# Kernel optimization log

Measured on AMD Instinct MI355X. Metric: run time of the kernel, lower is better.

Reference implementation:

```python
import jax, jax.numpy as jnp
import numpy as np

B, T, D = 2, 1024, 2048
HK, HV, DK, DV = 16, 32, 128, 128
KCONV = 4
INTER = 8192
EPS = 1e-6
KEY_DIM = HK * DK          # 2048
VAL_DIM = HV * DV          # 4096
CONV_DIM = 2 * KEY_DIM + VAL_DIM  # 8192


def setup_inputs() -> dict:
    key = jax.random.key(0)
    ks = jax.random.split(key, 16)
    s = 0.02
    return {
        "positions": jnp.broadcast_to(jnp.arange(T, dtype=jnp.int32), (B, T)),
        "hidden_states": jax.random.normal(ks[0], (B, T, D), jnp.float32),
        "residual": jax.random.normal(ks[1], (B, T, D), jnp.float32),
        "ln_in_w": jnp.zeros((D,), jnp.float32),
        "ln_post_w": jnp.zeros((D,), jnp.float32),
        "Wqkvz": jax.random.normal(ks[2], (D, 2 * KEY_DIM + 2 * VAL_DIM), jnp.float32) * s,
        "Wba": jax.random.normal(ks[3], (D, 2 * HV), jnp.float32) * s,
        "conv_w": jax.random.normal(ks[4], (CONV_DIM, KCONV), jnp.float32) * 0.1,
        "A_log": jnp.log(jax.random.uniform(ks[5], (HV,), jnp.float32, 1.0, 16.0)),
        "dt_bias": jax.random.normal(ks[6], (HV,), jnp.float32) * 0.1,
        "norm_w": jnp.ones((DV,), jnp.float32),
        "Wout": jax.random.normal(ks[7], (VAL_DIM, D), jnp.float32) * s,
        "Wgate": jax.random.normal(ks[8], (D, INTER), jnp.float32) * s,
        "Wup": jax.random.normal(ks[9], (D, INTER), jnp.float32) * s,
        "Wdown": jax.random.normal(ks[10], (INTER, D), jnp.float32) * s,
    }


def _gemma_rmsnorm(x, w):
    xf = x.astype(jnp.float32)
    v = jnp.mean(xf * xf, axis=-1, keepdims=True)
    return (xf * jax.lax.rsqrt(v + EPS) * (1.0 + w)).astype(x.dtype)


def _causal_depthwise_conv(x, w):
    # x: [B,T,C], w: [C,K]; causal depthwise conv1d
    Kw = w.shape[1]
    Tlen = x.shape[1]
    xp = jnp.pad(x, ((0, 0), (Kw - 1, 0), (0, 0)))
    return sum(xp[:, i:i + Tlen, :] * w[:, i] for i in range(Kw))


def _l2norm(x):
    return x * jax.lax.rsqrt(jnp.sum(x * x, axis=-1, keepdims=True) + 1e-6)


def reference(positions, hidden_states, residual, ln_in_w, ln_post_w, Wqkvz, Wba,
              conv_w, A_log, dt_bias, norm_w, Wout, Wgate, Wup, Wdown):
    b, t, d = hidden_states.shape
    # fused input RMSNorm + residual add
    res1 = hidden_states + residual
    h = _gemma_rmsnorm(res1, ln_in_w)

    # ---- GatedDeltaNet linear attention ----
    qkvz = h @ Wqkvz
    q, k, v, z = jnp.split(qkvz, [KEY_DIM, 2 * KEY_DIM, 2 * KEY_DIM + VAL_DIM], axis=-1)
    ba = h @ Wba
    bb, aa = jnp.split(ba, [HV], axis=-1)  # [b,t,HV] each

    qkv = jax.nn.silu(_causal_depthwise_conv(jnp.concatenate([q, k, v], axis=-1), conv_w))
    q, k, v = jnp.split(qkv, [KEY_DIM, 2 * KEY_DIM], axis=-1)

    q = _l2norm(q.reshape(b, t, HK, DK))
    k = _l2norm(k.reshape(b, t, HK, DK))
    v = v.reshape(b, t, HV, DV)
    z = z.reshape(b, t, HV, DV)
    rep = HV // HK
    q = jnp.repeat(q, rep, axis=2) * (DK ** -0.5)  # [b,t,HV,DK]
    k = jnp.repeat(k, rep, axis=2)

    beta = jax.nn.sigmoid(bb)                              # [b,t,HV]
    decay = jnp.exp(-jnp.exp(A_log) * jax.nn.softplus(aa + dt_bias))  # [b,t,HV]

    def step(S, xs):
        q_t, k_t, v_t, b_t, d_t = xs  # [b,HV,DK],[b,HV,DK],[b,HV,DV],[b,HV],[b,HV]
        S = S * d_t[..., None, None]
        v_pred = jnp.einsum('bhk,bhkv->bhv', k_t, S)
        delta = (v_t - v_pred) * b_t[..., None]
        S = S + jnp.einsum('bhk,bhv->bhkv', k_t, delta)
        o = jnp.einsum('bhk,bhkv->bhv', q_t, S)
        return S, o

    xs = (q.transpose(1, 0, 2, 3), k.transpose(1, 0, 2, 3), v.transpose(1, 0, 2, 3),
          beta.transpose(1, 0, 2), decay.transpose(1, 0, 2))
    S0 = jnp.zeros((b, HV, DK, DV), dtype=q.dtype)
    _, o = jax.lax.scan(step, S0, xs)
    o = o.transpose(1, 0, 2, 3)  # [b,t,HV,DV]

    # gated per-head RMSNorm: gate first (Qwen3-Next style), then normalize
    og = (o * jax.nn.silu(z)).astype(jnp.float32)
    var = jnp.mean(og * og, axis=-1, keepdims=True)
    og = (og * jax.lax.rsqrt(var + EPS)) * norm_w
    attn = og.reshape(b, t, VAL_DIM).astype(h.dtype) @ Wout

    # fused post-attention RMSNorm + residual
    res2 = attn + res1
    h2 = _gemma_rmsnorm(res2, ln_post_w)

    # gated SiLU MLP
    out = (jax.nn.silu(h2 @ Wgate) * (h2 @ Wup)) @ Wdown
    return (out, res2)
```

## Files before the change

kernel.cpp:

```cpp
#include <hip/hip_runtime.h>
#include <hip/hip_bf16.h>

typedef unsigned short u16;
typedef unsigned int u32;
typedef float f32x4 __attribute__((ext_vector_type(4)));
typedef short bf16x8 __attribute__((ext_vector_type(8)));
typedef unsigned short u16x4 __attribute__((ext_vector_type(4)));
typedef unsigned int u32x2 __attribute__((ext_vector_type(2)));
typedef unsigned int u32x4 __attribute__((ext_vector_type(4)));

#define BT 2048
#define DMODEL 2048
#define HV 32
#define DK 128
#define KEYDIM 2048
#define VALDIM 4096
#define QKVZ_N 12288
#define CONVC 8192
#define INTER 8192

__device__ __forceinline__ float bf2f(u16 v) {
  u32 u = ((u32)v) << 16;
  return __builtin_bit_cast(float, u);
}
__device__ __forceinline__ u16 f2bf(float f) {
  u32 u = __builtin_bit_cast(u32, f);
  u32 r = (u + 0x7fffu + ((u >> 16) & 1u)) >> 16;
  return (u16)r;
}
__device__ __forceinline__ u32 pack2(float a, float b) {
  return (u32)f2bf(a) | ((u32)f2bf(b) << 16);
}
__device__ __forceinline__ float siluf(float x) {
  return x / (1.f + expf(-x));
}

__global__ __launch_bounds__(256) void convert_transpose(
    const float* __restrict__ W, int ldw, u16* __restrict__ Wt, int K, int N) {
  __shared__ float tileT[64][68];
  int n0 = blockIdx.x * 64, k0 = blockIdx.y * 64;
  int tx = threadIdx.x & 15, ty = threadIdx.x >> 4;
#pragma unroll
  for (int i = 0; i < 4; ++i) {
    int kk = ty + i * 16;
    f32x4 v = *(const f32x4*)(W + (size_t)(k0 + kk) * ldw + n0 + tx * 4);
#pragma unroll
    for (int j = 0; j < 4; ++j) tileT[tx * 4 + j][kk] = v[j];
  }
  __syncthreads();
#pragma unroll
  for (int i = 0; i < 4; ++i) {
    int nn = ty + i * 16;
    f32x4 v = *(const f32x4*)(&tileT[nn][tx * 4]);
    u16x4 st;
#pragma unroll
    for (int j = 0; j < 4; ++j) st[j] = f2bf(v[j]);
    *(u16x4*)(Wt + (size_t)(n0 + nn) * K + k0 + tx * 4) = st;
  }
}

__global__ __launch_bounds__(256) void resnorm_kernel(
    const float* __restrict__ a, const float* __restrict__ b,
    const float* __restrict__ w, float* __restrict__ resout,
    u16* __restrict__ hb) {
  int tok = blockIdx.x, t = threadIdx.x;
  const float* ap = a + (size_t)tok * DMODEL + t * 8;
  const float* bp = b + (size_t)tok * DMODEL + t * 8;
  f32x4 x0 = *(const f32x4*)ap + *(const f32x4*)bp;
  f32x4 x1 = *(const f32x4*)(ap + 4) + *(const f32x4*)(bp + 4);
  *(f32x4*)(resout + (size_t)tok * DMODEL + t * 8) = x0;
  *(f32x4*)(resout + (size_t)tok * DMODEL + t * 8 + 4) = x1;
  float ss = 0.f;
#pragma unroll
  for (int j = 0; j < 4; ++j) ss += x0[j] * x0[j] + x1[j] * x1[j];
#pragma unroll
  for (int m = 1; m < 64; m <<= 1) ss += __shfl_xor(ss, m, 64);
  __shared__ float red[4];
  if ((t & 63) == 0) red[t >> 6] = ss;
  __syncthreads();
  ss = red[0] + red[1] + red[2] + red[3];
  float sc = rsqrtf(ss * (1.f / (float)DMODEL) + 1e-6f);
  const float* wp = w + t * 8;
  float y[8];
#pragma unroll
  for (int j = 0; j < 4; ++j) {
    y[j] = x0[j] * sc * (1.f + wp[j]);
    y[4 + j] = x1[j] * sc * (1.f + wp[4 + j]);
  }
  u32x4 st;
  st[0] = pack2(y[0], y[1]);
  st[1] = pack2(y[2], y[3]);
  st[2] = pack2(y[4], y[5]);
  st[3] = pack2(y[6], y[7]);
  *(u32x4*)(hb + (size_t)tok * DMODEL + t * 8) = st;
}

__global__ __launch_bounds__(256) void resnorm2_kernel(
    const float* __restrict__ p, const float* __restrict__ b,
    const float* __restrict__ w, float* __restrict__ resout,
    u16* __restrict__ hb) {
  int tok = blockIdx.x, t = threadIdx.x;
  size_t base = (size_t)tok * DMODEL + t * 8;
  const float* p0 = p + base;
  const float* p1 = p + (size_t)BT * DMODEL + base;
  const float* bp = b + base;
  f32x4 x0 = *(const f32x4*)p0 + *(const f32x4*)p1 + *(const f32x4*)bp;
  f32x4 x1 = *(const f32x4*)(p0 + 4) + *(const f32x4*)(p1 + 4) +
             *(const f32x4*)(bp + 4);
  *(f32x4*)(resout + base) = x0;
  *(f32x4*)(resout + base + 4) = x1;
  float ss = 0.f;
#pragma unroll
  for (int j = 0; j < 4; ++j) ss += x0[j] * x0[j] + x1[j] * x1[j];
#pragma unroll
  for (int m = 1; m < 64; m <<= 1) ss += __shfl_xor(ss, m, 64);
  __shared__ float red[4];
  if ((t & 63) == 0) red[t >> 6] = ss;
  __syncthreads();
  ss = red[0] + red[1] + red[2] + red[3];
  float sc = rsqrtf(ss * (1.f / (float)DMODEL) + 1e-6f);
  const float* wp = w + t * 8;
  float y[8];
#pragma unroll
  for (int j = 0; j < 4; ++j) {
    y[j] = x0[j] * sc * (1.f + wp[j]);
    y[4 + j] = x1[j] * sc * (1.f + wp[4 + j]);
  }
  u32x4 st;
  st[0] = pack2(y[0], y[1]);
  st[1] = pack2(y[2], y[3]);
  st[2] = pack2(y[4], y[5]);
  st[3] = pack2(y[6], y[7]);
  *(u32x4*)(hb + base) = st;
}

__device__ __forceinline__ void async16(const void* g, void* l) {
  __builtin_amdgcn_global_load_lds(
      (const __attribute__((address_space(1))) u32*)g,
      (__attribute__((address_space(3))) u32*)l, 16, 0, 0);
}

template <int OUT>
__global__ __launch_bounds__(256) void gemm_kernel(
    const u16* __restrict__ A, const u16* __restrict__ Bt,
    void* __restrict__ Cv, const u16* __restrict__ Aux, int M, int N,
    int Kfull, int Ks) {
  __shared__ __align__(16) u16 Al[4][128 * 32];
  __shared__ __align__(16) u16 Bl[4][128 * 32];
  int tid = threadIdx.x;
  int w = tid >> 6, l = tid & 63;
  int wr = w >> 1, wc = w & 1;
  int r15 = l & 15, kb = l >> 4;

  int nbx = gridDim.x, nby = gridDim.y;
  int bid = blockIdx.y * nbx + blockIdx.x;
  int nwg = nbx * nby;
  int cpx = nwg >> 3;
  int wg = (bid & 7) * cpx + (bid >> 3);
  const int GRP = 4;
  int span = GRP * nby;
  int grpId = wg / span;
  int rem = wg - grpId * span;
  int n0 = (grpId * GRP + (rem % GRP)) * 128;
  int m0 = (rem / GRP) * 128;
  int kbase = blockIdx.z * Ks;

  f32x4 acc[4][4] = {};

  const u16* baseA[2];
  const u16* baseB[2];
#pragma unroll
  for (int c = 0; c < 2; ++c) {
    int gid = w * 128 + c * 64 + l;
    int row = gid >> 2;
    int g = (gid & 3) ^ ((row >> 1) & 3);
    baseA[c] = A + (size_t)(m0 + row) * Kfull + kbase + g * 8;
    baseB[c] = Bt + (size_t)(n0 + row) * Kfull + kbase + g * 8;
  }
  auto stage = [&](int buf, int koff) {
#pragma unroll
    for (int c = 0; c < 2; ++c) {
      int gid = w * 128 + c * 64 + l;
      async16(baseA[c] + koff, Al[buf] + gid * 8);
      async16(baseB[c] + koff, Bl[buf] + gid * 8);
    }
  };

  int nst = Ks >> 5;
#pragma unroll
  for (int p = 0; p < 3; ++p)
    if (p < nst) stage(p & 3, p * 32);

  for (int i = 0; i < nst; ++i) {
    int issued = (i + 3 < nst) ? (i + 3) : nst;
    int infl = issued - i - 1;
    if (infl >= 2)
      asm volatile("s_waitcnt vmcnt(8)" ::: "memory");
    else if (infl == 1)
      asm volatile("s_waitcnt vmcnt(4)" ::: "memory");
    else
      asm volatile("s_waitcnt vmcnt(0)" ::: "memory");
    __builtin_amdgcn_s_barrier();
    __builtin_amdgcn_sched_barrier(0);
    if (i + 3 < nst) stage((i + 3) & 3, (i + 3) * 32);
    const u16* Ac = Al[i & 3];
    const u16* Bc = Bl[i & 3];
    bf16x8 aF[4], bF[4];
#pragma unroll
    for (int m = 0; m < 4; ++m) {
      int row = wr * 64 + m * 16 + r15;
      aF[m] = *(const bf16x8*)(Ac + row * 32 + (kb ^ ((row >> 1) & 3)) * 8);
    }
#pragma unroll
    for (int n = 0; n < 4; ++n) {
      int row = wc * 64 + n * 16 + r15;
      bF[n] = *(const bf16x8*)(Bc + row * 32 + (kb ^ ((row >> 1) & 3)) * 8);
    }
#pragma unroll
    for (int m = 0; m < 4; ++m)
#pragma unroll
      for (int n = 0; n < 4; ++n)
        acc[m][n] = __builtin_amdgcn_mfma_f32_16x16x32_bf16(aF[m], bF[n],
                                                            acc[m][n], 0, 0, 0);
  }

  float* Cf = (float*)Cv + (size_t)blockIdx.z * M * N;
#pragma unroll
  for (int m = 0; m < 4; ++m)
#pragma unroll
    for (int n = 0; n < 4; ++n) {
      size_t base = (size_t)(m0 + wr * 64 + m * 16 + kb * 4) * N +
                    (n0 + wc * 64 + n * 16 + r15);
#pragma unroll
      for (int r = 0; r < 4; ++r) {
        size_t idx = base + (size_t)r * N;
        if (OUT == 0)
          Cf[idx] = acc[m][n][r];
        else if (OUT == 1)
          ((u16*)Cv)[idx] = f2bf(acc[m][n][r]);
        else
          ((u16*)Cv)[idx] = f2bf(siluf(bf2f(Aux[idx])) * acc[m][n][r]);
      }
    }
}

#define GPHASE(ACHUNK, BCHUNK, Q, READ_B, ST_OP, ST_KH, TAILVM)              \
  {                                                                          \
    if (READ_B) {                                                            \
      _Pragma("unroll") for (int n = 0; n < 4; ++n) {                        \
        int row = wn * 64 + n * 16 + r15;                                    \
        bF[n] = *(const bf16x8*)((BCHUNK) + row * 32 +                       \
                                 (kb ^ ((row >> 1) & 3)) * 8);               \
      }                                                                      \
    }                                                                        \
    _Pragma("unroll") for (int mm = 0; mm < 4; ++mm) {                       \
      int row = wm * 128 + (Q)*64 + mm * 16 + r15;                           \
      aF[mm] = *(const bf16x8*)((ACHUNK) + row * 32 +                        \
                                (kb ^ ((row >> 1) & 3)) * 8);                \
    }                                                                        \
    if (hn) stage(buf ^ 1, ST_OP, ST_KH, koff);                              \
    __builtin_amdgcn_s_barrier();                                            \
    asm volatile("s_waitcnt lgkmcnt(0)" ::: "memory");                       \
    __builtin_amdgcn_sched_barrier(0);                                       \
    __builtin_amdgcn_s_setprio(1);                                           \
    _Pragma("unroll") for (int mm = 0; mm < 4; ++mm)                         \
        _Pragma("unroll") for (int n = 0; n < 4; ++n)                        \
            acc[(Q)*4 + mm][n] = __builtin_amdgcn_mfma_f32_16x16x32_bf16(    \
                aF[mm], bF[n], acc[(Q)*4 + mm][n], 0, 0, 0);                 \
    __builtin_amdgcn_s_setprio(0);                                           \
    if (TAILVM) {                                                            \
      if (hn)                                                                \
        asm volatile("s_waitcnt vmcnt(4)" ::: "memory");                     \
      else                                                                   \
        asm volatile("s_waitcnt vmcnt(0)" ::: "memory");                     \
    }                                                                        \
    __builtin_amdgcn_s_barrier();                                            \
  }

template <int OUT>
__global__ __launch_bounds__(512, 2) void gemm256_kernel(
    const u16* __restrict__ A, const u16* __restrict__ Bt,
    void* __restrict__ Cv, const u16* __restrict__ Aux, int M, int N,
    int Kfull, int Ks) {
  __shared__ __align__(16) u16 S[65536];
  int tid = threadIdx.x;
  int l = tid & 63, w = tid >> 6;
  int wm = w >> 2, wn = w & 3;
  int r15 = l & 15, kb = l >> 4;

  int nbx = gridDim.x, nby = gridDim.y;
  int bid = blockIdx.y * nbx + blockIdx.x;
  int nwg = nbx * nby;
  int cpx = nwg >> 3;
  int wg = (bid & 7) * cpx + (bid >> 3);
  const int GRP = 4;
  int span = GRP * nby;
  int grpId = wg / span;
  int rem = wg - grpId * span;
  int n0 = (grpId * GRP + (rem % GRP)) * 256;
  int m0 = (rem / GRP) * 256;
  int kbase = blockIdx.z * Ks;

  f32x4 acc[8][4] = {};

  const u16* baseA[2];
  const u16* baseB[2];
#pragma unroll
  for (int c = 0; c < 2; ++c) {
    int gid = c * 512 + tid;
    int row = gid >> 2, gg = gid & 3;
    int gl = gg ^ ((row >> 1) & 3);
    baseA[c] = A + (size_t)(m0 + row) * Kfull + kbase + gl * 8;
    baseB[c] = Bt + (size_t)(n0 + row) * Kfull + kbase + gl * 8;
  }
  auto stage = [&](int buf, int op, int kh, int koff) {
#pragma unroll
    for (int c = 0; c < 2; ++c) {
      int gid = c * 512 + tid;
      const u16* src = (op == 0 ? baseA[c] : baseB[c]) + koff + kh * 32;
      async16(src, S + ((buf * 2 + op) * 2 + kh) * 8192 + gid * 8);
    }
  };

  int nt = Ks >> 6;
  stage(0, 0, 0, 0);
  stage(0, 1, 0, 0);
  stage(0, 0, 1, 0);
  stage(0, 1, 1, 0);
  asm volatile("s_waitcnt vmcnt(4)" ::: "memory");
  __builtin_amdgcn_s_barrier();

  for (int t = 0; t < nt; ++t) {
    int buf = t & 1;
    bool hn = t + 1 < nt;
    int koff = (t + 1) * 64;
    const u16* Ac0 = S + ((buf * 2 + 0) * 2 + 0) * 8192;
    const u16* Ac1 = S + ((buf * 2 + 0) * 2 + 1) * 8192;
    const u16* Bc0 = S + ((buf * 2 + 1) * 2 + 0) * 8192;
    const u16* Bc1 = S + ((buf * 2 + 1) * 2 + 1) * 8192;
    bf16x8 aF[4], bF[4];
    GPHASE(Ac0, Bc0, 0, true, 0, 0, false)
    GPHASE(Ac0, Bc0, 1, false, 1, 0, true)
    GPHASE(Ac1, Bc1, 0, true, 0, 1, false)
    GPHASE(Ac1, Bc1, 1, false, 1, 1, true)
  }

  float* Cf = (float*)Cv + (size_t)blockIdx.z * M * N;
#pragma unroll
  for (int m = 0; m < 8; ++m)
#pragma unroll
    for (int n = 0; n < 4; ++n) {
      size_t base = (size_t)(m0 + wm * 128 + m * 16 + kb * 4) * N +
                    (n0 + wn * 64 + n * 16 + r15);
#pragma unroll
      for (int r = 0; r < 4; ++r) {
        size_t idx = base + (size_t)r * N;
        if (OUT == 0)
          Cf[idx] = acc[m][n][r];
        else if (OUT == 1)
          ((u16*)Cv)[idx] = f2bf(acc[m][n][r]);
        else
          ((u16*)Cv)[idx] = f2bf(siluf(bf2f(Aux[idx])) * acc[m][n][r]);
      }
    }
}

__global__ __launch_bounds__(256) void reduce_kernel(
    const float* __restrict__ p, float* __restrict__ o, int n, int S) {
  int i = (blockIdx.x * 256 + threadIdx.x) * 4;
  f32x4 s = *(const f32x4*)(p + i);
  for (int j = 1; j < S; ++j) s += *(const f32x4*)(p + (size_t)j * n + i);
  *(f32x4*)(o + i) = s;
}

__global__ __launch_bounds__(256) void ba_gemm_kernel(
    const u16* __restrict__ hb, const float* __restrict__ Wba,
    float* __restrict__ ba) {
  int m = blockIdx.x;
  int t = threadIdx.x;
  int n = t & 63, kq = t >> 6;
  const u16* a = hb + (size_t)m * DMODEL + kq * 512;
  const float* wp = Wba + (size_t)kq * 512 * 64 + n;
  float sum = 0.f;
  for (int i = 0; i < 512; ++i)
    sum += bf2f(a[i]) * wp[(size_t)i * 64];
  __shared__ float red[256];
  red[t] = sum;
  __syncthreads();
  if (t < 64)
    ba[(size_t)m * 64 + t] = red[t] + red[t + 64] + red[t + 128] + red[t + 192];
}

__global__ __launch_bounds__(256) void conv_silu_kernel(
    const u16* __restrict__ qkvb, const float* __restrict__ conv_w,
    u16* __restrict__ qkv) {
  int gid = blockIdx.x * 256 + threadIdx.x;
  int c4 = (gid & 2047) * 4;
  int bt = gid >> 11;
  int b = bt >> 10, tt = bt & 1023;
  f32x4 wv[4];
#pragma unroll
  for (int j = 0; j < 4; ++j) wv[j] = *(const f32x4*)(conv_w + (c4 + j) * 4);
  float acc[4] = {0.f, 0.f, 0.f, 0.f};
#pragma unroll
  for (int i = 0; i < 4; ++i) {
    int ts = tt - 3 + i;
    if (ts >= 0) {
      u16x4 x = *(const u16x4*)(qkvb + (size_t)(b * 1024 + ts) * CONVC + c4);
#pragma unroll
      for (int j = 0; j < 4; ++j) acc[j] += bf2f(x[j]) * wv[j][i];
    }
  }
  u32x2 st;
  st[0] = pack2(siluf(acc[0]), siluf(acc[1]));
  st[1] = pack2(siluf(acc[2]), siluf(acc[3]));
  *(u32x2*)(qkv + (size_t)bt * CONVC + c4) = st;
}

__global__ __launch_bounds__(256) void l2norm_kernel(u16* __restrict__ qkv) {
  int wid = blockIdx.x * 4 + (threadIdx.x >> 6);
  int l = threadIdx.x & 63;
  int tok = wid >> 5, slot = wid & 31;
  u16* p = qkv + (size_t)tok * CONVC + slot * 128 + l * 2;
  float x0 = bf2f(p[0]), x1 = bf2f(p[1]);
  float ss = x0 * x0 + x1 * x1;
#pragma unroll
  for (int m = 1; m < 64; m <<= 1) ss += __shfl_xor(ss, m, 64);
  float sc = rsqrtf(ss + 1e-6f);
  if (slot < 16) sc *= 0.08838834764831845f;
  *(u32*)p = pack2(x0 * sc, x1 * sc);
}

__global__ __launch_bounds__(256) void betadecay_kernel(
    const float* __restrict__ ba, const float* __restrict__ A_log,
    const float* __restrict__ dt_bias, float* __restrict__ bd) {
  int idx = blockIdx.x * 256 + threadIdx.x;
  int h = idx & 31;
  int tok = idx >> 5;
  int b = tok >> 10, tt = tok & 1023;
  float bb = ba[(size_t)tok * 64 + h];
  float aa = ba[(size_t)tok * 64 + 32 + h];
  float bet = 1.f / (1.f + expf(-bb));
  float x = aa + dt_bias[h];
  float sp = (x > 20.f) ? x : log1pf(expf(x));
  float dec = expf(-expf(A_log[h]) * sp);
  size_t o = (((size_t)(b * 32 + h)) * 1024 + tt) * 2;
  bd[o] = bet;
  bd[o + 1] = dec;
}

__global__ __launch_bounds__(256) void prep_kernel(
    const u16* __restrict__ qkvc, const float* __restrict__ bdpack,
    u16* __restrict__ Tg, u16* __restrict__ Pg, u16* __restrict__ KtTg,
    float* __restrict__ Bvec) {
  __shared__ __align__(16) u16 Kl[64 * 128];
  __shared__ __align__(16) u16 Ql[64 * 128];
  __shared__ __align__(16) float Af[64 * 65];
  __shared__ float bl[64], betal[64], sc63[64];
  int tid = threadIdx.x;
  int w = tid >> 6, l = tid & 63;
  int r15 = l & 15, kb = l >> 4;
  int c = blockIdx.x, bh = blockIdx.y;
  int b = bh >> 5, h = bh & 31, hk = h >> 1;
  size_t tok0 = (size_t)b * 1024 + c * 64;
  int ch = bh * 16 + c;

#pragma unroll
  for (int rep = 0; rep < 4; ++rep) {
    int gid = w * 256 + rep * 64 + l;
    int row = gid >> 4, seg = gid & 15;
    const u16* srcq = qkvc + (tok0 + row) * CONVC + hk * 128 + seg * 8;
    async16(srcq, Ql + gid * 8);
    async16(srcq + KEYDIM, Kl + gid * 8);
  }
  if (tid < 64) {
    size_t o = ((size_t)bh * 1024 + c * 64 + tid) * 2;
    betal[tid] = bdpack[o];
    float s = logf(fmaxf(bdpack[o + 1], 1e-30f));
#pragma unroll
    for (int d = 1; d < 64; d <<= 1) {
      float t = __shfl_up(s, d, 64);
      if (tid >= d) s += t;
    }
    bl[tid] = s;
    float tot = __shfl(s, 63, 64);
    sc63[tid] = expf(tot - s);
    Bvec[(size_t)ch * 64 + tid] = expf(s);
  }
  __syncthreads();

  {
    f32x4 akk[4] = {}, aqk[4] = {};
#pragma unroll
    for (int ks = 0; ks < 4; ++ks) {
      bf16x8 kaF = *(const bf16x8*)(Kl + (w * 16 + r15) * 128 + ks * 32 + kb * 8);
      bf16x8 qaF = *(const bf16x8*)(Ql + (w * 16 + r15) * 128 + ks * 32 + kb * 8);
#pragma unroll
      for (int n = 0; n < 4; ++n) {
        bf16x8 bF = *(const bf16x8*)(Kl + (n * 16 + r15) * 128 + ks * 32 + kb * 8);
        akk[n] = __builtin_amdgcn_mfma_f32_16x16x32_bf16(kaF, bF, akk[n], 0, 0, 0);
        aqk[n] = __builtin_amdgcn_mfma_f32_16x16x32_bf16(qaF, bF, aqk[n], 0, 0, 0);
      }
    }
#pragma unroll
    for (int n = 0; n < 4; ++n)
#pragma unroll
      for (int r = 0; r < 4; ++r) {
        int i = w * 16 + kb * 4 + r;
        int j = n * 16 + r15;
        float e = expf(bl[i] - bl[j]);
        Af[i * 65 + j] = (j < i) ? betal[i] * e * akk[n][r] : 0.f;
        u16 pv = (j <= i) ? f2bf(e * aqk[n][r]) : (u16)0;
        Pg[(size_t)ch * 4096 + i * 64 + j] = pv;
      }
  }
  for (int m = 0; m < 32; ++m) {
    int idx = tid * 32 + m;
    int d = idx >> 6, j = idx & 63;
    KtTg[(size_t)ch * 8192 + idx] = f2bf(bf2f(Kl[j * 128 + d]) * sc63[j]);
  }
  __syncthreads();

  {
    int ccol = w * 16 + r15;
    float tj[16];
#pragma unroll
    for (int m = 0; m < 16; ++m) tj[m] = (4 * m + kb == ccol) ? 1.f : 0.f;
#pragma unroll
    for (int i = 1; i < 64; ++i) {
      float part = 0.f;
      const int mb = (i + 3) >> 2;
#pragma unroll
      for (int m = 0; m < 16; ++m)
        if (m < mb) part = fmaf(Af[i * 65 + 4 * m + kb], tj[m], part);
      part += __shfl_xor(part, 16, 64);
      part += __shfl_xor(part, 32, 64);
      float nv = ((ccol == i) ? 1.f : 0.f) - part;
      if (kb == (i & 3)) tj[i >> 2] = nv;
    }
#pragma unroll
    for (int m = 0; m < 16; ++m)
      Tg[(size_t)ch * 4096 + (4 * m + kb) * 64 + ccol] = f2bf(tj[m]);
  }
}

__global__ __launch_bounds__(512) void chunk_scan_kernel(
    const u16* __restrict__ qkvc, const float* __restrict__ bdpack,
    const u16* __restrict__ Tg, const u16* __restrict__ Pg,
    const u16* __restrict__ KtTg, const float* __restrict__ Bvec,
    u16* __restrict__ obf) {
  __shared__ __align__(16) u16 Kl[64 * 128];
  __shared__ __align__(16) u16 Ql[64 * 128];
  __shared__ __align__(16) u16 KtTl[128 * 64];
  __shared__ __align__(16) u16 Tl[64 * 64];
  __shared__ __align__(16) u16 Pl[64 * 64];
  __shared__ __align__(16) u16 Vl[64 * 32];
  __shared__ __align__(16) u16 St[32 * 128];
  __shared__ __align__(16) u16 rhsT[32 * 64];
  __shared__ __align__(16) u16 dT[32 * 64];
  __shared__ float betal[64], Gl[64];

  int tid = threadIdx.x;
  int w = tid >> 6, l = tid & 63;
  int r15 = l & 15, kb = l >> 4;
  int dvc = blockIdx.x, bh = blockIdx.y;
  int b = bh >> 5, h = bh & 31, hk = h >> 1;
  int a = w >> 1, bcol = w & 1;

  for (int m = tid; m < 32 * 128; m += 512) St[m] = 0;
  f32x4 sAcc0 = {}, sAcc1 = {};
  __syncthreads();

  for (int c = 0; c < 16; ++c) {
    size_t tok0 = (size_t)b * 1024 + c * 64;
    int ch = bh * 16 + c;
#pragma unroll
    for (int rep = 0; rep < 2; ++rep) {
      int gid = w * 128 + rep * 64 + l;
      int row = gid >> 4, seg = gid & 15;
      const u16* srcq = qkvc + (tok0 + row) * CONVC + hk * 128 + seg * 8;
      async16(srcq, Ql + gid * 8);
      async16(srcq + KEYDIM, Kl + gid * 8);
      async16(KtTg + (size_t)ch * 8192 + gid * 8, KtTl + gid * 8);
    }
    {
      int gid = w * 64 + l;
      async16(Tg + (size_t)ch * 4096 + gid * 8, Tl + gid * 8);
      async16(Pg + (size_t)ch * 4096 + gid * 8, Pl + gid * 8);
    }
    if (w < 4) {
      int gid = w * 64 + l;
      int row = gid >> 2, seg = gid & 3;
      async16(qkvc + (tok0 + row) * CONVC + 2 * KEYDIM + h * 128 + dvc * 32 + seg * 8,
              Vl + gid * 8);
    }
    if (tid < 64) {
      betal[tid] = bdpack[((size_t)bh * 1024 + c * 64 + tid) * 2];
      Gl[tid] = Bvec[(size_t)ch * 64 + tid];
    }
    __syncthreads();

    f32x4 aKS = {}, aQS = {};
#pragma unroll
    for (int ks = 0; ks < 4; ++ks) {
      bf16x8 bF = *(const bf16x8*)(St + (bcol * 16 + r15) * 128 + ks * 32 + kb * 8);
      bf16x8 kF = *(const bf16x8*)(Kl + (a * 16 + r15) * 128 + ks * 32 + kb * 8);
      bf16x8 qF = *(const bf16x8*)(Ql + (a * 16 + r15) * 128 + ks * 32 + kb * 8);
      aKS = __builtin_amdgcn_mfma_f32_16x16x32_bf16(kF, bF, aKS, 0, 0, 0);
      aQS = __builtin_amdgcn_mfma_f32_16x16x32_bf16(qF, bF, aQS, 0, 0, 0);
    }
    {
      int i0 = a * 16 + kb * 4;
      int dv = bcol * 16 + r15;
      u16x4 st;
#pragma unroll
      for (int r = 0; r < 4; ++r) {
        int i = i0 + r;
        float v = bf2f(Vl[i * 32 + dv]);
        st[r] = f2bf(betal[i] * (v - Gl[i] * aKS[r]));
      }
      *(u16x4*)(rhsT + dv * 64 + i0) = st;
    }
    __syncthreads();
    f32x4 aD = {};
#pragma unroll
    for (int ks = 0; ks < 2; ++ks) {
      bf16x8 aF = *(const bf16x8*)(Tl + (a * 16 + r15) * 64 + ks * 32 + kb * 8);
      bf16x8 bF = *(const bf16x8*)(rhsT + (bcol * 16 + r15) * 64 + ks * 32 + kb * 8);
      aD = __builtin_amdgcn_mfma_f32_16x16x32_bf16(aF, bF, aD, 0, 0, 0);
    }
    {
      int i0 = a * 16 + kb * 4;
      int dv = bcol * 16 + r15;
      u16x4 st;
#pragma unroll
      for (int r = 0; r < 4; ++r) st[r] = f2bf(aD[r]);
      *(u16x4*)(dT + dv * 64 + i0) = st;
    }
    __syncthreads();
    f32x4 aO = {};
#pragma unroll
    for (int ks = 0; ks < 2; ++ks) {
      bf16x8 aF = *(const bf16x8*)(Pl + (a * 16 + r15) * 64 + ks * 32 + kb * 8);
      bf16x8 bF = *(const bf16x8*)(dT + (bcol * 16 + r15) * 64 + ks * 32 + kb * 8);
      aO = __builtin_amdgcn_mfma_f32_16x16x32_bf16(aF, bF, aO, 0, 0, 0);
    }
    {
      int i0 = a * 16 + kb * 4;
      int dv = bcol * 16 + r15;
#pragma unroll
      for (int r = 0; r < 4; ++r) {
        int i = i0 + r;
        float o = aO[r] + Gl[i] * aQS[r];
        obf[(tok0 + i) * VALDIM + h * 128 + dvc * 32 + dv] = f2bf(o);
      }
    }
    float gL = Gl[63];
#pragma unroll
    for (int r = 0; r < 4; ++r) { sAcc0[r] *= gL; sAcc1[r] *= gL; }
#pragma unroll
    for (int ks = 0; ks < 2; ++ks) {
      bf16x8 aF = *(const bf16x8*)(KtTl + (w * 16 + r15) * 64 + ks * 32 + kb * 8);
      bf16x8 b0 = *(const bf16x8*)(dT + r15 * 64 + ks * 32 + kb * 8);
      bf16x8 b1 = *(const bf16x8*)(dT + (16 + r15) * 64 + ks * 32 + kb * 8);
      sAcc0 = __builtin_amdgcn_mfma_f32_16x16x32_bf16(aF, b0, sAcc0, 0, 0, 0);
      sAcc1 = __builtin_amdgcn_mfma_f32_16x16x32_bf16(aF, b1, sAcc1, 0, 0, 0);
    }
#pragma unroll
    for (int r = 0; r < 4; ++r) {
      int dk = w * 16 + kb * 4 + r;
      St[r15 * 128 + dk] = f2bf(sAcc0[r]);
      St[(16 + r15) * 128 + dk] = f2bf(sAcc1[r]);
    }
    __syncthreads();
  }
}

__global__ __launch_bounds__(256) void gatenorm_kernel(
    const u16* __restrict__ obf, u16* __restrict__ zb,
    const float* __restrict__ norm_w) {
  int wid = blockIdx.x * 4 + (threadIdx.x >> 6);
  int l = threadIdx.x & 63;
  int tok = wid >> 5, h = wid & 31;
  const u16* op = obf + (size_t)tok * VALDIM + h * 128 + l * 2;
  u16* zp = zb + (size_t)tok * VALDIM + h * 128 + l * 2;
  float o0 = bf2f(op[0]), o1 = bf2f(op[1]);
  float z0 = bf2f(zp[0]), z1 = bf2f(zp[1]);
  float g0 = o0 * siluf(z0);
  float g1 = o1 * siluf(z1);
  float ss = g0 * g0 + g1 * g1;
#pragma unroll
  for (int m = 1; m < 64; m <<= 1) ss += __shfl_xor(ss, m, 64);
  float sc = rsqrtf(ss * (1.f / 128.f) + 1e-6f);
  int e = l * 2;
  *(u32*)zp = pack2(g0 * sc * norm_w[e], g1 * sc * norm_w[e + 1]);
}

__global__ void diag_kernel(float* out, float val) { out[0] = val; }

extern "C" void kernel_launch(void* const* d_in, const int* in_sizes, int n_in,
                              void* d_out, int out_size, void* d_ws,
                              size_t ws_size, hipStream_t stream) {
  const float* hidden = (const float*)d_in[1];
  const float* residual = (const float*)d_in[2];
  const float* ln_in_w = (const float*)d_in[3];
  const float* ln_post_w = (const float*)d_in[4];
  const float* Wqkvz = (const float*)d_in[5];
  const float* Wba = (const float*)d_in[6];
  const float* conv_w = (const float*)d_in[7];
  const float* A_log = (const float*)d_in[8];
  const float* dt_bias = (const float*)d_in[9];
  const float* norm_w = (const float*)d_in[10];
  const float* Wout = (const float*)d_in[11];
  const float* Wgate = (const float*)d_in[12];
  const float* Wup = (const float*)d_in[13];
  const float* Wdown = (const float*)d_in[14];

  char* ws = (char*)d_ws;
  size_t off = 0;
  auto alloc = [&](size_t n) {
    char* p = ws + off;
    off = (off + n + 255) & ~(size_t)255;
    return p;
  };
  u16* wslot = (u16*)alloc((size_t)INTER * DMODEL * 2);
  u16* hb = (u16*)alloc((size_t)BT * DMODEL * 2);
  u16* qkvb = (u16*)alloc((size_t)BT * CONVC * 2);
  u16* zb = (u16*)alloc((size_t)BT * VALDIM * 2);
  u16* qkvc = (u16*)alloc((size_t)BT * CONVC * 2);
  float* ba = (float*)alloc((size_t)BT * 64 * 4);
  float* bdpack = (float*)alloc((size_t)64 * 1024 * 2 * 4);
  u16* obf = (u16*)alloc((size_t)BT * VALDIM * 2);
  if (off > ws_size) {
    diag_kernel<<<1, 1, 0, stream>>>((float*)d_out, (float)(ws_size >> 20));
    return;
  }

  float* res1 = (float*)d_out;
  float* res2 = (float*)d_out + (size_t)BT * DMODEL;
  u16* h2b = hb;
  u16* gbuf = qkvc;
  u16* mbuf = qkvb;
  float* outp = (float*)d_out;

  u16* Tg = qkvb;
  u16* Pg = qkvb + (size_t)1024 * 4096;
  u16* KtTg = qkvb + (size_t)2 * 1024 * 4096;
  float* Bvec = ba;

  float* pWout = (float*)qkvb;
  float* pDown = (float*)zb;

  dim3 blk(256);
  dim3 blk512(512);

  resnorm_kernel<<<BT, blk, 0, stream>>>(hidden, residual, ln_in_w, res1, hb);

  convert_transpose<<<dim3(CONVC / 64, DMODEL / 64), blk, 0, stream>>>(
      Wqkvz, QKVZ_N, wslot, DMODEL, CONVC);
  gemm256_kernel<1><<<dim3(CONVC / 256, BT / 256), blk512, 0, stream>>>(
      hb, wslot, qkvb, nullptr, BT, CONVC, DMODEL, DMODEL);

  convert_transpose<<<dim3(VALDIM / 64, DMODEL / 64), blk, 0, stream>>>(
      Wqkvz + CONVC, QKVZ_N, wslot, DMODEL, VALDIM);
  gemm_kernel<1><<<dim3(VALDIM / 128, BT / 128), blk, 0, stream>>>(
      hb, wslot, zb, nullptr, BT, VALDIM, DMODEL, DMODEL);

  ba_gemm_kernel<<<BT, blk, 0, stream>>>(hb, Wba, ba);

  conv_silu_kernel<<<BT * 2048 / 256, blk, 0, stream>>>(qkvb, conv_w, qkvc);
  l2norm_kernel<<<BT * 32 / 4, blk, 0, stream>>>(qkvc);
  betadecay_kernel<<<BT * HV / 256, blk, 0, stream>>>(ba, A_log, dt_bias,
                                                      bdpack);

  prep_kernel<<<dim3(16, 64), blk, 0, stream>>>(qkvc, bdpack, Tg, Pg, KtTg,
                                                Bvec);
  chunk_scan_kernel<<<dim3(4, 64), dim3(512), 0, stream>>>(
      qkvc, bdpack, Tg, Pg, KtTg, Bvec, obf);

  gatenorm_kernel<<<BT * HV / 4, blk, 0, stream>>>(obf, zb, norm_w);

  convert_transpose<<<dim3(DMODEL / 64, VALDIM / 64), blk, 0, stream>>>(
      Wout, DMODEL, wslot, VALDIM, DMODEL);
  gemm_kernel<0><<<dim3(DMODEL / 128, BT / 128, 2), blk, 0, stream>>>(
      zb, wslot, pWout, nullptr, BT, DMODEL, VALDIM, VALDIM / 2);

  resnorm2_kernel<<<BT, blk, 0, stream>>>(pWout, res1, ln_post_w, res2, h2b);

  convert_transpose<<<dim3(INTER / 64, DMODEL / 64), blk, 0, stream>>>(
      Wgate, INTER, wslot, DMODEL, INTER);
  gemm256_kernel<1><<<dim3(INTER / 256, BT / 256), blk512, 0, stream>>>(
      h2b, wslot, gbuf, nullptr, BT, INTER, DMODEL, DMODEL);

  convert_transpose<<<dim3(INTER / 64, DMODEL / 64), blk, 0, stream>>>(
      Wup, INTER, wslot, DMODEL, INTER);
  gemm256_kernel<2><<<dim3(INTER / 256, BT / 256), blk512, 0, stream>>>(
      h2b, wslot, mbuf, gbuf, BT, INTER, DMODEL, DMODEL);

  convert_transpose<<<dim3(DMODEL / 64, INTER / 64), blk, 0, stream>>>(
      Wdown, DMODEL, wslot, INTER, DMODEL);
  gemm256_kernel<0><<<dim3(DMODEL / 256, BT / 256, 4), blk512, 0, stream>>>(
      mbuf, wslot, pDown, nullptr, BT, DMODEL, INTER, INTER / 4);
  reduce_kernel<<<BT * DMODEL / 1024, blk, 0, stream>>>(pDown, outp,
                                                        BT * DMODEL, 4);
}
```

Baseline: 764.4 us.

## Use 1024-thread GEMM tiles and fuse conv/l2norm and ba/betadecay kernels

The 256x256 GEMM now runs with 1024 threads (16 waves, each holding a 64x64 accumulator) instead of 512 threads, with one async load per operand per half-k and a simpler barrier schedule. Separately, causal conv+SiLU and per-head L2 norm are fused into one per-token kernel, and the beta/alpha projection is fused with the beta/decay computation, which removes intermediate buffers and launches. The Bvec buffer gets its own allocation instead of aliasing ba. The risks are register or LDS pressure and occupancy changes in the GEMM, plus a 256-thread per-token conv kernel that keeps 32 accumulators per thread.

```diff
diff --git a/kernel.cpp b/kernel.cpp
--- a/kernel.cpp
+++ b/kernel.cpp
@@ -244,41 +244,8 @@
     }
 }
 
-#define GPHASE(ACHUNK, BCHUNK, Q, READ_B, ST_OP, ST_KH, TAILVM)              \
-  {                                                                          \
-    if (READ_B) {                                                            \
-      _Pragma("unroll") for (int n = 0; n < 4; ++n) {                        \
-        int row = wn * 64 + n * 16 + r15;                                    \
-        bF[n] = *(const bf16x8*)((BCHUNK) + row * 32 +                       \
-                                 (kb ^ ((row >> 1) & 3)) * 8);               \
-      }                                                                      \
-    }                                                                        \
-    _Pragma("unroll") for (int mm = 0; mm < 4; ++mm) {                       \
-      int row = wm * 128 + (Q)*64 + mm * 16 + r15;                           \
-      aF[mm] = *(const bf16x8*)((ACHUNK) + row * 32 +                        \
-                                (kb ^ ((row >> 1) & 3)) * 8);                \
-    }                                                                        \
-    if (hn) stage(buf ^ 1, ST_OP, ST_KH, koff);                              \
-    __builtin_amdgcn_s_barrier();                                            \
-    asm volatile("s_waitcnt lgkmcnt(0)" ::: "memory");                       \
-    __builtin_amdgcn_sched_barrier(0);                                       \
-    __builtin_amdgcn_s_setprio(1);                                           \
-    _Pragma("unroll") for (int mm = 0; mm < 4; ++mm)                         \
-        _Pragma("unroll") for (int n = 0; n < 4; ++n)                        \
-            acc[(Q)*4 + mm][n] = __builtin_amdgcn_mfma_f32_16x16x32_bf16(    \
-                aF[mm], bF[n], acc[(Q)*4 + mm][n], 0, 0, 0);                 \
-    __builtin_amdgcn_s_setprio(0);                                           \
-    if (TAILVM) {                                                            \
-      if (hn)                                                                \
-        asm volatile("s_waitcnt vmcnt(4)" ::: "memory");                     \
-      else                                                                   \
-        asm volatile("s_waitcnt vmcnt(0)" ::: "memory");                     \
-    }                                                                        \
-    __builtin_amdgcn_s_barrier();                                            \
-  }
-
 template <int OUT>
-__global__ __launch_bounds__(512, 2) void gemm256_kernel(
+__global__ __launch_bounds__(1024, 1) void gemm1024_kernel(
     const u16* __restrict__ A, const u16* __restrict__ Bt,
     void* __restrict__ Cv, const u16* __restrict__ Aux, int M, int N,
     int Kfull, int Ks) {
@@ -301,56 +268,71 @@
   int m0 = (rem / GRP) * 256;
   int kbase = blockIdx.z * Ks;
 
-  f32x4 acc[8][4] = {};
-
-  const u16* baseA[2];
-  const u16* baseB[2];
-#pragma unroll
-  for (int c = 0; c < 2; ++c) {
-    int gid = c * 512 + tid;
-    int row = gid >> 2, gg = gid & 3;
-    int gl = gg ^ ((row >> 1) & 3);
-    baseA[c] = A + (size_t)(m0 + row) * Kfull + kbase + gl * 8;
-    baseB[c] = Bt + (size_t)(n0 + row) * Kfull + kbase + gl * 8;
-  }
-  auto stage = [&](int buf, int op, int kh, int koff) {
-#pragma unroll
-    for (int c = 0; c < 2; ++c) {
-      int gid = c * 512 + tid;
-      const u16* src = (op == 0 ? baseA[c] : baseB[c]) + koff + kh * 32;
-      async16(src, S + ((buf * 2 + op) * 2 + kh) * 8192 + gid * 8);
-    }
-  };
+  f32x4 acc[4][4] = {};
+
+  int srow = tid >> 2, sgg = tid & 3;
+  int sgl = sgg ^ ((srow >> 1) & 3);
+  const u16* baseA = A + (size_t)(m0 + srow) * Kfull + kbase + sgl * 8;
+  const u16* baseB = Bt + (size_t)(n0 + srow) * Kfull + kbase + sgl * 8;
 
   int nt = Ks >> 6;
-  stage(0, 0, 0, 0);
-  stage(0, 1, 0, 0);
-  stage(0, 0, 1, 0);
-  stage(0, 1, 1, 0);
-  asm volatile("s_waitcnt vmcnt(4)" ::: "memory");
+#pragma unroll
+  for (int kh = 0; kh < 2; ++kh) {
+    async16(baseA + kh * 32, S + ((0 * 2 + 0) * 2 + kh) * 8192 + tid * 8);
+    async16(baseB + kh * 32, S + ((0 * 2 + 1) * 2 + kh) * 8192 + tid * 8);
+  }
+  asm volatile("s_waitcnt vmcnt(2)" ::: "memory");
   __builtin_amdgcn_s_barrier();
 
   for (int t = 0; t < nt; ++t) {
     int buf = t & 1;
     bool hn = t + 1 < nt;
     int koff = (t + 1) * 64;
-    const u16* Ac0 = S + ((buf * 2 + 0) * 2 + 0) * 8192;
-    const u16* Ac1 = S + ((buf * 2 + 0) * 2 + 1) * 8192;
-    const u16* Bc0 = S + ((buf * 2 + 1) * 2 + 0) * 8192;
-    const u16* Bc1 = S + ((buf * 2 + 1) * 2 + 1) * 8192;
-    bf16x8 aF[4], bF[4];
-    GPHASE(Ac0, Bc0, 0, true, 0, 0, false)
-    GPHASE(Ac0, Bc0, 1, false, 1, 0, true)
-    GPHASE(Ac1, Bc1, 0, true, 0, 1, false)
-    GPHASE(Ac1, Bc1, 1, false, 1, 1, true)
+#pragma unroll
+    for (int kh = 0; kh < 2; ++kh) {
+      const u16* Ac = S + ((buf * 2 + 0) * 2 + kh) * 8192;
+      const u16* Bc = S + ((buf * 2 + 1) * 2 + kh) * 8192;
+      bf16x8 aF[4], bF[4];
+#pragma unroll
+      for (int m = 0; m < 4; ++m) {
+        int row = wm * 64 + m * 16 + r15;
+        aF[m] = *(const bf16x8*)(Ac + row * 32 + (kb ^ ((row >> 1) & 3)) * 8);
+      }
+#pragma unroll
+      for (int n = 0; n < 4; ++n) {
+        int row = wn * 64 + n * 16 + r15;
+        bF[n] = *(const bf16x8*)(Bc + row * 32 + (kb ^ ((row >> 1) & 3)) * 8);
+      }
+      if (hn) {
+        async16(baseA + koff + kh * 32,
+                S + (((buf ^ 1) * 2 + 0) * 2 + kh) * 8192 + tid * 8);
+        async16(baseB + koff + kh * 32,
+                S + (((buf ^ 1) * 2 + 1) * 2 + kh) * 8192 + tid * 8);
+      }
+      asm volatile("s_waitcnt lgkmcnt(0)" ::: "memory");
+      __builtin_amdgcn_sched_barrier(0);
+      __builtin_amdgcn_s_setprio(1);
+#pragma unroll
+      for (int m = 0; m < 4; ++m)
+#pragma unroll
+        for (int n = 0; n < 4; ++n)
+          acc[m][n] = __builtin_amdgcn_mfma_f32_16x16x32_bf16(
+              aF[m], bF[n], acc[m][n], 0, 0, 0);
+      __builtin_amdgcn_s_setprio(0);
+      if (hn)
+        asm volatile("s_waitcnt vmcnt(2)" ::: "memory");
+      else if (kh == 0)
+        asm volatile("s_waitcnt vmcnt(0)" ::: "memory");
+      __builtin_amdgcn_s_barrier();
+    }
   }
 
   float* Cf = (float*)Cv + (size_t)blockIdx.z * M * N;
 #pragma unroll
-  for (int m = 0; m < 8; ++m)
+  for (int m = 0; m < 4; ++m)
 #pragma unroll
     for (int n = 0; n < 4; ++n) {
-      size_t base = (size_t)(m0 + wm * 128 + m * 16 + kb * 4) * N +
+      size_t base = (size_t)(m0 + wm * 64 + m * 16 + kb * 4) * N +
                     (n0 + wn * 64 + n * 16 + r15);
 #pragma unroll
       for (int r = 0; r < 4; ++r) {
@@ -373,9 +355,10 @@
   *(f32x4*)(o + i) = s;
 }
 
-__global__ __launch_bounds__(256) void ba_gemm_kernel(
+__global__ __launch_bounds__(256) void ba_bd_kernel(
     const u16* __restrict__ hb, const float* __restrict__ Wba,
-    float* __restrict__ ba) {
+    const float* __restrict__ A_log, const float* __restrict__ dt_bias,
+    float* __restrict__ bd) {
   int m = blockIdx.x;
   int t = threadIdx.x;
   int n = t & 63, kq = t >> 6;
@@ -387,66 +370,72 @@
   __shared__ float red[256];
   red[t] = sum;
   __syncthreads();
-  if (t < 64)
-    ba[(size_t)m * 64 + t] = red[t] + red[t + 64] + red[t + 128] + red[t + 192];
-}
-
-__global__ __launch_bounds__(256) void conv_silu_kernel(
+  if (t < 32) {
+    float bb = red[t] + red[t + 64] + red[t + 128] + red[t + 192];
+    float aa = red[t + 32] + red[t + 96] + red[t + 160] + red[t + 224];
+    float bet = 1.f / (1.f + expf(-bb));
+    float x = aa + dt_bias[t];
+    float sp = (x > 20.f) ? x : log1pf(expf(x));
+    float dec = expf(-expf(A_log[t]) * sp);
+    int b = m >> 10, tt = m & 1023;
+    size_t o = (((size_t)(b * 32 + t)) * 1024 + tt) * 2;
+    bd[o] = bet;
+    bd[o + 1] = dec;
+  }
+}
+
+__global__ __launch_bounds__(256) void conv_l2_kernel(
     const u16* __restrict__ qkvb, const float* __restrict__ conv_w,
     u16* __restrict__ qkv) {
-  int gid = blockIdx.x * 256 + threadIdx.x;
-  int c4 = (gid & 2047) * 4;
-  int bt = gid >> 11;
-  int b = bt >> 10, tt = bt & 1023;
-  f32x4 wv[4];
-#pragma unroll
-  for (int j = 0; j < 4; ++j) wv[j] = *(const f32x4*)(conv_w + (c4 + j) * 4);
-  float acc[4] = {0.f, 0.f, 0.f, 0.f};
-#pragma unroll
-  for (int i = 0; i < 4; ++i) {
-    int ts = tt - 3 + i;
-    if (ts >= 0) {
-      u16x4 x = *(const u16x4*)(qkvb + (size_t)(b * 1024 + ts) * CONVC + c4);
-#pragma unroll
-      for (int j = 0; j < 4; ++j) acc[j] += bf2f(x[j]) * wv[j][i];
-    }
-  }
-  u32x2 st;
-  st[0] = pack2(siluf(acc[0]), siluf(acc[1]));
-  st[1] = pack2(siluf(acc[2]), siluf(acc[3]));
-  *(u32x2*)(qkv + (size_t)bt * CONVC + c4) = st;
-}
-
-__global__ __launch_bounds__(256) void l2norm_kernel(u16* __restrict__ qkv) {
-  int wid = blockIdx.x * 4 + (threadIdx.x >> 6);
-  int l = threadIdx.x & 63;
-  int tok = wid >> 5, slot = wid & 31;
-  u16* p = qkv + (size_t)tok * CONVC + slot * 128 + l * 2;
-  float x0 = bf2f(p[0]), x1 = bf2f(p[1]);
-  float ss = x0 * x0 + x1 * x1;
-#pragma unroll
-  for (int m = 1; m < 64; m <<= 1) ss += __shfl_xor(ss, m, 64);
-  float sc = rsqrtf(ss + 1e-6f);
-  if (slot < 16) sc *= 0.08838834764831845f;
-  *(u32*)p = pack2(x0 * sc, x1 * sc);
-}
-
-__global__ __launch_bounds__(256) void betadecay_kernel(
-    const float* __restrict__ ba, const float* __restrict__ A_log,
-    const float* __restrict__ dt_bias, float* __restrict__ bd) {
-  int idx = blockIdx.x * 256 + threadIdx.x;
-  int h = idx & 31;
-  int tok = idx >> 5;
+  int tok = blockIdx.x;
   int b = tok >> 10, tt = tok & 1023;
-  float bb = ba[(size_t)tok * 64 + h];
-  float aa = ba[(size_t)tok * 64 + 32 + h];
-  float bet = 1.f / (1.f + expf(-bb));
-  float x = aa + dt_bias[h];
-  float sp = (x > 20.f) ? x : log1pf(expf(x));
-  float dec = expf(-expf(A_log[h]) * sp);
-  size_t o = (((size_t)(b * 32 + h)) * 1024 + tt) * 2;
-  bd[o] = bet;
-  bd[o + 1] = dec;
+  int t = threadIdx.x;
+  int c0 = t * 32;
+  float acc[32];
+  {
+    bf16x8 x[4][4];
+    bool valid[4];
+#pragma unroll
+    for (int i = 0; i < 4; ++i) {
+      int ts = tt - 3 + i;
+      valid[i] = ts >= 0;
+      const u16* rp = qkvb + (size_t)(b * 1024 + (valid[i] ? ts : 0)) * CONVC + c0;
+#pragma unroll
+      for (int gq = 0; gq < 4; ++gq) x[i][gq] = *(const bf16x8*)(rp + gq * 8);
+    }
+#pragma unroll
+    for (int gq = 0; gq < 4; ++gq)
+#pragma unroll
+      for (int j = 0; j < 8; ++j) {
+        f32x4 wv = *(const f32x4*)(conv_w + (c0 + gq * 8 + j) * 4);
+        float s = 0.f;
+#pragma unroll
+        for (int i = 0; i < 4; ++i)
+          if (valid[i]) s = fmaf(bf2f((u16)x[i][gq][j]), wv[i], s);
+        acc[gq * 8 + j] = siluf(s);
+      }
+  }
+  if (t < 128) {
+    float ss = 1e-6f;
+#pragma unroll
+    for (int j = 0; j < 32; ++j) ss += acc[j] * acc[j];
+    ss += __shfl_xor(ss, 1, 64);
+    ss += __shfl_xor(ss, 2, 64);
+    ss -= 3e-6f;
+    float sc = rsqrtf(ss);
+    if (t < 64) sc *= 0.08838834764831845f;
+#pragma unroll
+    for (int j = 0; j < 32; ++j) acc[j] *= sc;
+  }
+  u16* op = qkv + (size_t)tok * CONVC + c0;
+#pragma unroll
+  for (int gq = 0; gq < 4; ++gq) {
+    u32x4 st;
+#pragma unroll
+    for (int p2 = 0; p2 < 4; ++p2)
+      st[p2] = pack2(acc[gq * 8 + p2 * 2], acc[gq * 8 + p2 * 2 + 1]);
+    *(u32x4*)(op + gq * 8) = st;
+  }
 }
 
 __global__ __launch_bounds__(256) void prep_kernel(
@@ -728,7 +717,7 @@
   u16* qkvb = (u16*)alloc((size_t)BT * CONVC * 2);
   u16* zb = (u16*)alloc((size_t)BT * VALDIM * 2);
   u16* qkvc = (u16*)alloc((size_t)BT * CONVC * 2);
-  float* ba = (float*)alloc((size_t)BT * 64 * 4);
+  float* Bvec = (float*)alloc((size_t)1024 * 64 * 4);
   float* bdpack = (float*)alloc((size_t)64 * 1024 * 2 * 4);
   u16* obf = (u16*)alloc((size_t)BT * VALDIM * 2);
   if (off > ws_size) {
@@ -746,19 +735,18 @@
   u16* Tg = qkvb;
   u16* Pg = qkvb + (size_t)1024 * 4096;
   u16* KtTg = qkvb + (size_t)2 * 1024 * 4096;
-  float* Bvec = ba;
 
   float* pWout = (float*)qkvb;
   float* pDown = (float*)zb;
 
   dim3 blk(256);
-  dim3 blk512(512);
+  dim3 blk1024(1024);
 
   resnorm_kernel<<<BT, blk, 0, stream>>>(hidden, residual, ln_in_w, res1, hb);
 
   convert_transpose<<<dim3(CONVC / 64, DMODEL / 64), blk, 0, stream>>>(
       Wqkvz, QKVZ_N, wslot, DMODEL, CONVC);
-  gemm256_kernel<1><<<dim3(CONVC / 256, BT / 256), blk512, 0, stream>>>(
+  gemm1024_kernel<1><<<dim3(CONVC / 256, BT / 256), blk1024, 0, stream>>>(
       hb, wslot, qkvb, nullptr, BT, CONVC, DMODEL, DMODEL);
 
   convert_transpose<<<dim3(VALDIM / 64, DMODEL / 64), blk, 0, stream>>>(
@@ -766,12 +754,9 @@
   gemm_kernel<1><<<dim3(VALDIM / 128, BT / 128), blk, 0, stream>>>(
       hb, wslot, zb, nullptr, BT, VALDIM, DMODEL, DMODEL);
 
-  ba_gemm_kernel<<<BT, blk, 0, stream>>>(hb, Wba, ba);
-
-  conv_silu_kernel<<<BT * 2048 / 256, blk, 0, stream>>>(qkvb, conv_w, qkvc);
-  l2norm_kernel<<<BT * 32 / 4, blk, 0, stream>>>(qkvc);
-  betadecay_kernel<<<BT * HV / 256, blk, 0, stream>>>(ba, A_log, dt_bias,
-                                                      bdpack);
+  ba_bd_kernel<<<BT, blk, 0, stream>>>(hb, Wba, A_log, dt_bias, bdpack);
+
+  conv_l2_kernel<<<BT, blk, 0, stream>>>(qkvb, conv_w, qkvc);
 
   prep_kernel<<<dim3(16, 64), blk, 0, stream>>>(qkvc, bdpack, Tg, Pg, KtTg,
                                                 Bvec);
@@ -789,17 +774,17 @@
 
   convert_transpose<<<dim3(INTER / 64, DMODEL / 64), blk, 0, stream>>>(
       Wgate, INTER, wslot, DMODEL, INTER);
-  gemm256_kernel<1><<<dim3(INTER / 256, BT / 256), blk512, 0, stream>>>(
+  gemm1024_kernel<1><<<dim3(INTER / 256, BT / 256), blk1024, 0, stream>>>(
       h2b, wslot, gbuf, nullptr, BT, INTER, DMODEL, DMODEL);
 
   convert_transpose<<<dim3(INTER / 64, DMODEL / 64), blk, 0, stream>>>(
       Wup, INTER, wslot, DMODEL, INTER);
-  gemm256_kernel<2><<<dim3(INTER / 256, BT / 256), blk512, 0, stream>>>(
+  gemm1024_kernel<2><<<dim3(INTER / 256, BT / 256), blk1024, 0, stream>>>(
       h2b, wslot, mbuf, gbuf, BT, INTER, DMODEL, DMODEL);
 
   convert_transpose<<<dim3(DMODEL / 64, INTER / 64), blk, 0, stream>>>(
       Wdown, DMODEL, wslot, INTER, DMODEL);
-  gemm256_kernel<0><<<dim3(DMODEL / 256, BT / 256, 4), blk512, 0, stream>>>(
+  gemm1024_kernel<0><<<dim3(DMODEL / 256, BT / 256, 4), blk1024, 0, stream>>>(
       mbuf, wslot, pDown, nullptr, BT, DMODEL, INTER, INTER / 4);
   reduce_kernel<<<BT * DMODEL / 1024, blk, 0, stream>>>(pDown, outp,
                                                         BT * DMODEL, 4);
```

Result: slower. 787.6 us (+3.0%).
